# Kernel optimization log

Hardware: AMD Instinct MI355X
Metric: run time of the kernel (lower is better)

## Reference

```python
import jax, jax.numpy as jnp
import numpy as np

B, N, D, R = 2, 256, 128, 32

def _sh_l1(r):
    # e3nn-style component-normalized l=1 spherical harmonics of unit vectors
    return jnp.sqrt(3.0) * r

def _sh_l2(r):
    x, y, z = r[..., 0], r[..., 1], r[..., 2]
    c = jnp.sqrt(15.0)
    return jnp.stack([
        c * x * y,
        c * y * z,
        0.5 * jnp.sqrt(5.0) * (3.0 * z * z - 1.0),  # x^2+y^2+z^2 = 1
        c * x * z,
        0.5 * c * (x * x - y * y),
    ], axis=-1)

def _radial(rbf, w1, b1, w2, b2):
    h = rbf @ w1 + b1
    return (h * jax.nn.sigmoid(h)) @ w2 + b2  # Linear -> SiLU -> Linear

def _layernorm(x, g, b, eps=1e-5):
    m = jnp.mean(x, axis=-1, keepdims=True)
    v = jnp.var(x, axis=-1, keepdims=True)
    return (x - m) * jax.lax.rsqrt(v + eps) * g + b

def setup_inputs() -> dict:
    key = jax.random.key(0)
    ks = iter(jax.random.split(key, 40))
    def nrm(shape, s=1.0):
        return jax.random.normal(next(ks), shape, dtype=jnp.float32) * s
    r_hat = nrm((B, N, N, 3))
    r_hat = r_hat / (jnp.linalg.norm(r_hat, axis=-1, keepdims=True) + 1e-9)
    inp = {
        'node_s': nrm((B, N, D)),
        'node_v': nrm((B, N, 3, D)),
        'node_t': nrm((B, N, 5, D)),
        'rbf': jax.random.uniform(next(ks), (B, N, N, R), dtype=jnp.float32),
        'r_hat': r_hat,
        'mask': jnp.ones((B, N, N), dtype=jnp.float32),
    }
    s1, s2 = 1.0 / np.sqrt(R), 1.0 / np.sqrt(D)
    for p in ('r0', 'r1', 'r2', 'r110'):
        inp[p + '_w1'] = nrm((R, D), s1)
        inp[p + '_b1'] = jnp.zeros((D,), jnp.float32)
        inp[p + '_w2'] = nrm((D, D), s2)
        inp[p + '_b2'] = jnp.zeros((D,), jnp.float32)
    inp['src_w'] = nrm((D, D), s2)
    inp['ln_g'] = jnp.ones((D,), jnp.float32)
    inp['ln_b'] = jnp.zeros((D,), jnp.float32)
    inp['out_w'] = nrm((D, D), s2)
    inp['out_b'] = jnp.zeros((D,), jnp.float32)
    inp['v_scale'] = jnp.ones((D,), jnp.float32)
    inp['t_scale'] = jnp.ones((D,), jnp.float32)
    return inp

def reference(node_s, node_v, node_t, rbf, r_hat, mask,
              r0_w1, r0_b1, r0_w2, r0_b2,
              r1_w1, r1_b1, r1_w2, r1_b2,
              r2_w1, r2_b1, r2_w2, r2_b2,
              r110_w1, r110_b1, r110_w2, r110_b2,
              src_w, ln_g, ln_b, out_w, out_b, v_scale, t_scale):
    h = node_s @ src_w                               # (B,N,D)
    h_j = h[:, None, :, :] * mask[..., None]         # (B,N,N,D): h_j[b,i,j]=h[b,j]*mask[b,i,j]
    Y1 = _sh_l1(r_hat)                               # (B,N,N,3)
    Y2 = _sh_l2(r_hat)                               # (B,N,N,5)

    msg_s = jnp.sum(h_j * _radial(rbf, r0_w1, r0_b1, r0_w2, r0_b2), axis=2)  # (B,N,D)
    delta_v = jnp.einsum('bijd,bijc->bicd',
                         h_j * _radial(rbf, r1_w1, r1_b1, r1_w2, r1_b2), Y1) * v_scale
    delta_t = jnp.einsum('bijd,bijc->bicd',
                         h_j * _radial(rbf, r2_w1, r2_b1, r2_w2, r2_b2), Y2) * t_scale

    # v_j[b,i,j] = node_v[b,i] (per the torch unsqueeze(2).expand)
    dot_vY1 = jnp.einsum('bicd,bijc->bijd', node_v, Y1)                      # (B,N,N,D)
    msg_s_from_v = jnp.sum(dot_vY1 * _radial(rbf, r110_w1, r110_b1, r110_w2, r110_b2)
                           * mask[..., None], axis=2)                        # (B,N,D)

    delta_s = _layernorm(msg_s + msg_s_from_v, ln_g, ln_b) @ out_w + out_b
    return (delta_s, delta_v, delta_t)
```

## Files before the change

kernel.cpp:

```cpp
#include <hip/hip_runtime.h>

#define Bb 2
#define Nn 256
#define Dd 128
#define Rr 32

typedef unsigned short u16;
typedef unsigned int   u32;
typedef __attribute__((ext_vector_type(8))) short bf16x8;
typedef __attribute__((ext_vector_type(4))) short bf16x4;
typedef __attribute__((ext_vector_type(4))) float f32x4;
typedef __attribute__((ext_vector_type(2))) u32   u32x2;

__device__ u16 g_w1t[4*Dd*Rr];
__device__ u16 g_w2t[4*Dd*Dd];

__device__ __forceinline__ short f2bfs(float f){
  u32 u = __float_as_uint(f);
  u += 0x7FFFu + ((u >> 16) & 1u);
  return (short)(u >> 16);
}
__device__ __forceinline__ u16 f2bf(float f){
  u32 u = __float_as_uint(f);
  u += 0x7FFFu + ((u >> 16) & 1u);
  return (u16)(u >> 16);
}
__device__ __forceinline__ u32 cvtpk(float a, float b){
  u32 r;
  asm("v_cvt_pk_bf16_f32 %0, %1, %2" : "=v"(r) : "v"(a), "v"(b));
  return r;
}

__global__ __launch_bounds__(128) void prep_kernel(
    const float* __restrict__ node_s, const float* __restrict__ src_w,
    const float* __restrict__ r0w1, const float* __restrict__ r1w1,
    const float* __restrict__ r2w1, const float* __restrict__ r3w1,
    const float* __restrict__ r0w2, const float* __restrict__ r1w2,
    const float* __restrict__ r2w2, const float* __restrict__ r3w2,
    float* __restrict__ h_out)
{
  const int bx = blockIdx.x;
  const int t  = threadIdx.x;
  if (bx < Bb*Nn){
    __shared__ float s_row[Dd];
    s_row[t] = node_s[(size_t)bx*Dd + t];
    __syncthreads();
    float acc = 0.f;
    #pragma unroll 8
    for (int k=0;k<Dd;k++) acc += s_row[k]*src_w[k*Dd + t];
    h_out[(size_t)bx*Dd + t] = acc;
  } else {
    const int kb = bx - Bb*Nn;
    const int p  = kb >> 3, sl = kb & 7;
    const float* W1 = (p==0)?r0w1:(p==1)?r1w1:(p==2)?r2w1:r3w1;
    const float* W2 = (p==0)?r0w2:(p==1)?r1w2:(p==2)?r2w2:r3w2;
    u16* W1T = g_w1t + p*Dd*Rr;
    u16* W2T = g_w2t + p*Dd*Dd;
    #pragma unroll
    for (int it=0; it<4; it++){
      int idx = sl*512 + it*128 + t;
      W1T[idx] = f2bf(W1[(idx & 31)*Dd + (idx >> 5)]);
    }
    #pragma unroll
    for (int it=0; it<16; it++){
      int idx = sl*2048 + it*128 + t;
      W2T[idx] = f2bf(W2[(idx & 127)*Dd + (idx >> 7)]);
    }
  }
}

__global__ __launch_bounds__(512,4) void se3_mfma8(
    const float* __restrict__ node_v,
    const float* __restrict__ rbf,
    const float* __restrict__ r_hat,
    const float* __restrict__ maskp,
    const float* __restrict__ r0b1, const float* __restrict__ r0b2,
    const float* __restrict__ r1b1, const float* __restrict__ r1b2,
    const float* __restrict__ r2b1, const float* __restrict__ r2b2,
    const float* __restrict__ r3b1, const float* __restrict__ r3b2,
    const float* __restrict__ ln_g, const float* __restrict__ ln_b,
    const float* __restrict__ out_w, const float* __restrict__ out_b,
    const float* __restrict__ v_scale, const float* __restrict__ t_scale,
    const float* __restrict__ h_ws,
    float* __restrict__ out_s, float* __restrict__ out_v, float* __restrict__ out_t)
{
  __shared__ u16   s_rbf[Nn*36];
  __shared__ u16   s_hid[64*136];
  __shared__ u16   s_YT[10*264];
  __shared__ u16   s_Y1r[3*264];
  __shared__ u16   s_G[128*72];
  __shared__ float s_red[16*130];
  __shared__ float s_msg[Dd];
  __shared__ float s_xn[Dd];
  __shared__ float s_part[4*Dd];
  __shared__ float s_mv[2];

  const int tid  = threadIdx.x;
  const int bi   = blockIdx.x;
  const int b    = bi >> 8;
  const int lane = tid & 63;
  const int w    = tid >> 6;
  const int q    = lane >> 4;
  const int cc   = lane & 15;
  const int mpair= w & 1;
  const int dgrp = w >> 1;
  const int dbase= dgrp*32;

  if (tid < Nn){
    int j = tid;
    size_t pidx = (size_t)bi*Nn + j;
    float mk = maskp[pidx];
    float x = r_hat[pidx*3+0];
    float y = r_hat[pidx*3+1];
    float z = r_hat[pidx*3+2];
    const float SQ3=1.7320508075688772f;
    const float C15=3.8729833462074170f;
    const float C5H=1.1180339887498949f;
    float y1a=SQ3*x, y1b=SQ3*y, y1c=SQ3*z;
    s_YT[0*264+j]=f2bf(mk);
    s_YT[1*264+j]=f2bf(y1a*mk);
    s_YT[2*264+j]=f2bf(y1b*mk);
    s_YT[3*264+j]=f2bf(y1c*mk);
    s_YT[4*264+j]=f2bf(C15*x*y*mk);
    s_YT[5*264+j]=f2bf(C15*y*z*mk);
    s_YT[6*264+j]=f2bf(C5H*(3.f*z*z-1.f)*mk);
    s_YT[7*264+j]=f2bf(C15*x*z*mk);
    s_YT[8*264+j]=f2bf(0.5f*C15*(x*x-y*y)*mk);
    s_YT[9*264+j]=f2bf(mk);
    s_Y1r[0*264+j]=f2bf(y1a);
    s_Y1r[1*264+j]=f2bf(y1b);
    s_Y1r[2*264+j]=f2bf(y1c);
  }

  const float* rbf_blk = rbf + (size_t)bi*Nn*Rr;
  const float* hb      = h_ws + (size_t)b*Nn*Dd;

  for (int idx=tid; idx<Nn*Rr/2; idx+=512){
    int j = idx >> 4, r2 = (idx & 15)*2;
    const float* src = &rbf_blk[j*Rr + r2];
    float v0 = src[0], v1 = src[1];
    *(u32*)&s_rbf[j*36 + r2] = cvtpk(v0, v1);
  }

  bf16x8 vBf[2];
  {
    const float* nv = node_v + (size_t)bi*3*Dd;
    #pragma unroll
    for (int nt=0;nt<2;nt++){
      int dd = dbase+nt*16+cc;
      bf16x8 t = {0,0,0,0,0,0,0,0};
      if (q==0){
        t[0]=f2bfs(nv[0*Dd+dd]);
        t[1]=f2bfs(nv[1*Dd+dd]);
        t[2]=f2bfs(nv[2*Dd+dd]);
      }
      vBf[nt]=t;
    }
  }

  const f32x4 zf = {0.f,0.f,0.f,0.f};
  f32x4 accred[2] = {zf, zf};

  #pragma unroll 1
  for (int p=0;p<4;p++){
    const float* B1p = (p==0)?r0b1:(p==1)?r1b1:(p==2)?r2b1:r3b1;
    const float* B2p = (p==0)?r0b2:(p==1)?r1b2:(p==2)?r2b2:r3b2;
    const u16* W1T = g_w1t + p*Dd*Rr;
    const u16* W2T = g_w2t + p*Dd*Dd;
    const int lo = (p==0)?0:(p==1)?1:(p==2)?4:9;
    const int hi = (p==0)?0:(p==1)?3:(p==2)?8:9;
    const u32 gmask = (cc>=lo && cc<=hi) ? 0xFFFFFFFFu : 0u;
    const u16* ytrow = &s_YT[(cc<10?cc:9)*264];

    bf16x8 w1f[2];
    bf16x8 w2f[2][4];
    f32x4  b1v4[2];
    float  b2v[2];
    #pragma unroll
    for (int nt=0;nt<2;nt++){
      int dd = dbase+nt*16+cc;
      b1v4[nt] = *(const f32x4*)&B1p[dbase + nt*16 + q*4];
      b2v[nt]=B2p[dd];
      w1f[nt] = *(const bf16x8*)&W1T[dd*Rr + q*8];
      #pragma unroll
      for (int ks=0;ks<4;ks++)
        w2f[nt][ks] = *(const bf16x8*)&W2T[dd*Dd + ks*32 + q*8];
    }

    #pragma unroll 1
    for (int ch=0; ch<4; ch++){
      __syncthreads();
      #pragma unroll
      for (int jt=0;jt<2;jt++){
        const int jrow = (mpair*2+jt)*16 + cc;
        const u16* bp = &s_rbf[(ch*64 + jrow)*36 + q*8];
        bf16x4 lo4 = *(const bf16x4*)bp;
        bf16x4 hi4 = *(const bf16x4*)(bp+4);
        bf16x8 rbff = {lo4[0],lo4[1],lo4[2],lo4[3],hi4[0],hi4[1],hi4[2],hi4[3]};
        #pragma unroll
        for (int nt=0;nt<2;nt++){
          f32x4 hc = __builtin_amdgcn_mfma_f32_16x16x32_bf16(w1f[nt], rbff, zf, 0,0,0);
          float s[4];
          #pragma unroll
          for (int r=0;r<4;r++){
            float x  = hc[r] + b1v4[nt][r];
            float e  = __expf(-x);
            s[r]     = x*__builtin_amdgcn_rcpf(1.f+e);
          }
          u32x2 pk = { cvtpk(s[0], s[1]), cvtpk(s[2], s[3]) };
          *(u32x2*)&s_hid[jrow*136 + dbase + nt*16 + q*4] = pk;
        }
      }
      __syncthreads();
      #pragma unroll 1
      for (int mm=0;mm<2;mm++){
        const int m = mpair*2 + mm;
        bf16x8 af[4];
        #pragma unroll
        for (int ks=0;ks<4;ks++)
          af[ks] = *(const bf16x8*)&s_hid[(m*16+cc)*136 + ks*32 + q*8];

        f32x4 dotC[2];
        if (p==3){
          bf16x8 aY = {0,0,0,0,0,0,0,0};
          if (q==0){
            int j = ch*64 + m*16 + cc;
            aY[0]=(short)s_Y1r[0*264+j];
            aY[1]=(short)s_Y1r[1*264+j];
            aY[2]=(short)s_Y1r[2*264+j];
          }
          #pragma unroll
          for (int nt=0;nt<2;nt++)
            dotC[nt] = __builtin_amdgcn_mfma_f32_16x16x32_bf16(aY, vBf[nt], zf, 0,0,0);
        }

        #pragma unroll
        for (int nt=0;nt<2;nt++){
          f32x4 c2 = zf;
          #pragma unroll
          for (int ks=0;ks<4;ks++)
            c2 = __builtin_amdgcn_mfma_f32_16x16x32_bf16(af[ks], w2f[nt][ks], c2, 0,0,0);
          const int dd = dbase+nt*16+cc;
          float g[4];
          if (p<3){
            const float* hp = hb + (size_t)(ch*64 + m*16 + q*4)*Dd + dd;
            #pragma unroll
            for (int r=0;r<4;r++)
              g[r] = (c2[r]+b2v[nt]) * hp[(size_t)r*Dd];
          } else {
            #pragma unroll
            for (int r=0;r<4;r++)
              g[r] = (c2[r]+b2v[nt]) * dotC[nt][r];
          }
          u32x2 pk = { cvtpk(g[0], g[1]), cvtpk(g[2], g[3]) };
          *(u32x2*)&s_G[(size_t)(dd)*72 + m*16 + q*4] = pk;
        }
      }
      {
        bf16x8 aR = *(const bf16x8*)(ytrow + ch*64 + mpair*32 + q*8);
        u32* arp = (u32*)&aR;
        arp[0]&=gmask; arp[1]&=gmask; arp[2]&=gmask; arp[3]&=gmask;
        #pragma unroll
        for (int nt=0;nt<2;nt++){
          bf16x8 bG = *(const bf16x8*)&s_G[(size_t)(dbase + nt*16 + cc)*72 + mpair*32 + q*8];
          accred[nt] = __builtin_amdgcn_mfma_f32_16x16x32_bf16(aR, bG, accred[nt], 0,0,0);
        }
      }
    }
  }

  if (mpair){
    #pragma unroll
    for (int nt=0;nt<2;nt++){
      const int d = dbase + nt*16 + cc;
      #pragma unroll
      for (int r=0;r<4;r++)
        s_red[(q*4+r)*130 + d] = accred[nt][r];
    }
  }
  __syncthreads();
  if (!mpair){
    #pragma unroll
    for (int nt=0;nt<2;nt++){
      const int d = dbase + nt*16 + cc;
      #pragma unroll
      for (int r=0;r<4;r++){
        const int rw = q*4 + r;
        float val = accred[nt][r] + s_red[rw*130 + d];
        if (rw==0)      s_msg[d] = val;
        else if (rw<=3) out_v[(size_t)bi*3*Dd + (size_t)(rw-1)*Dd + d] = val*v_scale[d];
        else if (rw<=8) out_t[(size_t)bi*5*Dd + (size_t)(rw-4)*Dd + d] = val*t_scale[d];
        else if (rw==9) s_xn[d] = val;
      }
    }
  }
  __syncthreads();

  if (tid < 64){
    float a0=s_msg[tid]+s_xn[tid], a1=s_msg[tid+64]+s_xn[tid+64];
    float s1=a0+a1, s2=a0*a0+a1*a1;
    #pragma unroll
    for (int off=1;off<64;off<<=1){
      s1 += __shfl_xor(s1,off);
      s2 += __shfl_xor(s2,off);
    }
    if (tid==0){
      float m   = s1*(1.f/Dd);
      float var = fmaxf(s2*(1.f/Dd) - m*m, 0.f);
      s_mv[0]=m;
      s_mv[1]=rsqrtf(var+1e-5f);
    }
  }
  __syncthreads();
  if (tid < Dd){
    float msg = s_msg[tid]+s_xn[tid];
    s_xn[tid] = (msg - s_mv[0])*s_mv[1]*ln_g[tid] + ln_b[tid];
  }
  __syncthreads();

  {
    int dp = tid & 127, seg = tid >> 7;
    float pa = 0.f;
    #pragma unroll 8
    for (int k=seg*32;k<seg*32+32;k++)
      pa += s_xn[k]*out_w[k*Dd+dp];
    s_part[seg*Dd+dp]=pa;
  }
  __syncthreads();
  if (tid < Dd)
    out_s[(size_t)bi*Dd+tid] = s_part[tid]+s_part[Dd+tid]+s_part[2*Dd+tid]+s_part[3*Dd+tid]+out_b[tid];
}

extern "C" void kernel_launch(void* const* d_in, const int* in_sizes, int n_in,
                              void* d_out, int out_size, void* d_ws, size_t ws_size,
                              hipStream_t stream) {
  const float* node_s = (const float*)d_in[0];
  const float* node_v = (const float*)d_in[1];
  const float* rbf    = (const float*)d_in[3];
  const float* r_hat  = (const float*)d_in[4];
  const float* maskp  = (const float*)d_in[5];
  const float* r0w1=(const float*)d_in[6],  *r0b1=(const float*)d_in[7];
  const float* r0w2=(const float*)d_in[8],  *r0b2=(const float*)d_in[9];
  const float* r1w1=(const float*)d_in[10], *r1b1=(const float*)d_in[11];
  const float* r1w2=(const float*)d_in[12], *r1b2=(const float*)d_in[13];
  const float* r2w1=(const float*)d_in[14], *r2b1=(const float*)d_in[15];
  const float* r2w2=(const float*)d_in[16], *r2b2=(const float*)d_in[17];
  const float* r3w1=(const float*)d_in[18], *r3b1=(const float*)d_in[19];
  const float* r3w2=(const float*)d_in[20], *r3b2=(const float*)d_in[21];
  const float* src_w  =(const float*)d_in[22];
  const float* ln_g   =(const float*)d_in[23];
  const float* ln_b   =(const float*)d_in[24];
  const float* out_w  =(const float*)d_in[25];
  const float* out_b  =(const float*)d_in[26];
  const float* v_scale=(const float*)d_in[27];
  const float* t_scale=(const float*)d_in[28];

  float* h_ws = (float*)d_ws;
  float* out_s = (float*)d_out;
  float* out_v = out_s + (size_t)Bb*Nn*Dd;
  float* out_t = out_v + (size_t)Bb*Nn*3*Dd;

  prep_kernel<<<dim3(Bb*Nn + 32), dim3(128), 0, stream>>>(
      node_s, src_w,
      r0w1, r1w1, r2w1, r3w1, r0w2, r1w2, r2w2, r3w2,
      h_ws);
  se3_mfma8<<<dim3(Bb*Nn), dim3(512), 0, stream>>>(
      node_v, rbf, r_hat, maskp,
      r0b1,r0b2, r1b1,r1b2, r2b1,r2b2, r3b1,r3b2,
      ln_g, ln_b, out_w, out_b, v_scale, t_scale,
      h_ws, out_s, out_v, out_t);
}
```

Baseline: 187.4 us.

## Keep reduction operand in registers, double-buffer swizzled hidden tile, drop a barrier

The per-chunk edge-reduction MFMA now takes its B operand straight from registers. The j-row permutation of the second-layer GEMM is chosen so the output accumulator layout matches the reduction MFMA's B-operand layout, which removes the s_G shared-memory round trip. The hidden-activation tile is double-buffered with an XOR swizzle instead of padding, so one of the two barriers per chunk can be dropped. The prep kernel's transpose now reads coalesced and scatters its writes. Correctness depends on the register permutation exactly matching the MFMA operand layout, and the double buffer raises shared-memory use.

```diff
diff --git a/kernel.cpp b/kernel.cpp
--- a/kernel.cpp
+++ b/kernel.cpp
@@ -11,6 +11,7 @@
 typedef __attribute__((ext_vector_type(4))) short bf16x4;
 typedef __attribute__((ext_vector_type(4))) float f32x4;
 typedef __attribute__((ext_vector_type(2))) u32   u32x2;
+typedef __attribute__((ext_vector_type(4))) u32   u32x4;
 
 __device__ u16 g_w1t[4*Dd*Rr];
 __device__ u16 g_w2t[4*Dd*Dd];
@@ -29,6 +30,9 @@
   u32 r;
   asm("v_cvt_pk_bf16_f32 %0, %1, %2" : "=v"(r) : "v"(a), "v"(b));
   return r;
+}
+__device__ __forceinline__ int swz(int j){
+  return (j&3) | ((((j>>2)^(j>>3))&1)<<2);
 }
 
 __global__ __launch_bounds__(128) void prep_kernel(
@@ -58,18 +62,18 @@
     u16* W2T = g_w2t + p*Dd*Dd;
     #pragma unroll
     for (int it=0; it<4; it++){
-      int idx = sl*512 + it*128 + t;
-      W1T[idx] = f2bf(W1[(idx & 31)*Dd + (idx >> 5)]);
+      int in = sl*512 + it*128 + t;
+      W1T[(in & 127)*Rr + (in >> 7)] = f2bf(W1[in]);
     }
     #pragma unroll
     for (int it=0; it<16; it++){
-      int idx = sl*2048 + it*128 + t;
-      W2T[idx] = f2bf(W2[(idx & 127)*Dd + (idx >> 7)]);
-    }
-  }
-}
-
-__global__ __launch_bounds__(512,4) void se3_mfma8(
+      int in = sl*2048 + it*128 + t;
+      W2T[(in & 127)*Dd + (in >> 7)] = f2bf(W2[in]);
+    }
+  }
+}
+
+__global__ __launch_bounds__(512,4) void se3_mfma9(
     const float* __restrict__ node_v,
     const float* __restrict__ rbf,
     const float* __restrict__ r_hat,
@@ -85,10 +89,9 @@
     float* __restrict__ out_s, float* __restrict__ out_v, float* __restrict__ out_t)
 {
   __shared__ u16   s_rbf[Nn*36];
-  __shared__ u16   s_hid[64*136];
+  __shared__ u16   s_hid[2*64*128];
   __shared__ u16   s_YT[10*264];
   __shared__ u16   s_Y1r[3*264];
-  __shared__ u16   s_G[128*72];
   __shared__ float s_red[16*130];
   __shared__ float s_msg[Dd];
   __shared__ float s_xn[Dd];
@@ -158,8 +161,11 @@
     }
   }
 
+  __syncthreads();
+
   const f32x4 zf = {0.f,0.f,0.f,0.f};
   f32x4 accred[2] = {zf, zf};
+  int buf = 0;
 
   #pragma unroll 1
   for (int p=0;p<4;p++){
@@ -189,7 +195,6 @@
 
     #pragma unroll 1
     for (int ch=0; ch<4; ch++){
-      __syncthreads();
       #pragma unroll
       for (int jt=0;jt<2;jt++){
         const int jrow = (mpair*2+jt)*16 + cc;
@@ -208,26 +213,29 @@
             s[r]     = x*__builtin_amdgcn_rcpf(1.f+e);
           }
           u32x2 pk = { cvtpk(s[0], s[1]), cvtpk(s[2], s[3]) };
-          *(u32x2*)&s_hid[jrow*136 + dbase + nt*16 + q*4] = pk;
+          const int c0 = dgrp*4 + nt*2 + (q>>1);
+          *(u32x2*)&s_hid[buf*8192 + jrow*128 + ((c0 ^ swz(jrow))<<3) + (q&1)*4] = pk;
         }
       }
       __syncthreads();
-      #pragma unroll 1
+
+      u32 bB[2][4];
+      #pragma unroll
       for (int mm=0;mm<2;mm++){
-        const int m = mpair*2 + mm;
+        const int jp = mpair*32 + ((cc>>2)<<3) + mm*4 + (cc&3);
         bf16x8 af[4];
         #pragma unroll
         for (int ks=0;ks<4;ks++)
-          af[ks] = *(const bf16x8*)&s_hid[(m*16+cc)*136 + ks*32 + q*8];
+          af[ks] = *(const bf16x8*)&s_hid[buf*8192 + jp*128 + (((ks*4+q) ^ swz(jp))<<3)];
 
         f32x4 dotC[2];
         if (p==3){
           bf16x8 aY = {0,0,0,0,0,0,0,0};
           if (q==0){
-            int j = ch*64 + m*16 + cc;
-            aY[0]=(short)s_Y1r[0*264+j];
-            aY[1]=(short)s_Y1r[1*264+j];
-            aY[2]=(short)s_Y1r[2*264+j];
+            int jg = ch*64 + jp;
+            aY[0]=(short)s_Y1r[0*264+jg];
+            aY[1]=(short)s_Y1r[1*264+jg];
+            aY[2]=(short)s_Y1r[2*264+jg];
           }
           #pragma unroll
           for (int nt=0;nt<2;nt++)
@@ -243,7 +251,7 @@
           const int dd = dbase+nt*16+cc;
           float g[4];
           if (p<3){
-            const float* hp = hb + (size_t)(ch*64 + m*16 + q*4)*Dd + dd;
+            const float* hp = hb + (size_t)(ch*64 + mpair*32 + q*8 + mm*4)*Dd + dd;
             #pragma unroll
             for (int r=0;r<4;r++)
               g[r] = (c2[r]+b2v[nt]) * hp[(size_t)r*Dd];
@@ -252,20 +260,23 @@
             for (int r=0;r<4;r++)
               g[r] = (c2[r]+b2v[nt]) * dotC[nt][r];
           }
-          u32x2 pk = { cvtpk(g[0], g[1]), cvtpk(g[2], g[3]) };
-          *(u32x2*)&s_G[(size_t)(dd)*72 + m*16 + q*4] = pk;
+          bB[nt][mm*2+0] = cvtpk(g[0], g[1]);
+          bB[nt][mm*2+1] = cvtpk(g[2], g[3]);
         }
       }
+
       {
         bf16x8 aR = *(const bf16x8*)(ytrow + ch*64 + mpair*32 + q*8);
         u32* arp = (u32*)&aR;
         arp[0]&=gmask; arp[1]&=gmask; arp[2]&=gmask; arp[3]&=gmask;
         #pragma unroll
         for (int nt=0;nt<2;nt++){
-          bf16x8 bG = *(const bf16x8*)&s_G[(size_t)(dbase + nt*16 + cc)*72 + mpair*32 + q*8];
+          u32x4 bw = { bB[nt][0], bB[nt][1], bB[nt][2], bB[nt][3] };
+          bf16x8 bG = __builtin_bit_cast(bf16x8, bw);
           accred[nt] = __builtin_amdgcn_mfma_f32_16x16x32_bf16(aR, bG, accred[nt], 0,0,0);
         }
       }
+      buf ^= 1;
     }
   }
 
@@ -364,7 +375,7 @@
       node_s, src_w,
       r0w1, r1w1, r2w1, r3w1, r0w2, r1w2, r2w2, r3w2,
       h_ws);
-  se3_mfma8<<<dim3(Bb*Nn), dim3(512), 0, stream>>>(
+  se3_mfma9<<<dim3(Bb*Nn), dim3(512), 0, stream>>>(
       node_v, rbf, r_hat, maskp,
       r0b1,r0b2, r1b1,r1b2, r2b1,r2b2, r3b1,r3b2,
       ln_g, ln_b, out_w, out_b, v_scale, t_scale,
```

Result: slower. 192.0 us (+2.5%).
